# Kernel tuning notes

Measured on AMD Instinct MI355X. Metric: run time of the kernel, lower is better.

Reference implementation:

```python
import jax, jax.numpy as jnp
import numpy as np

B, C, N, K_NN = 16, 64, 2048, 3
OUT_C = 64


def setup_inputs() -> dict:
    key = jax.random.key(0)
    k1, k2, k3 = jax.random.split(key, 3)
    x = jax.random.normal(k1, (B, C, N), dtype=jnp.float32)
    fan_in = C * K_NN
    bound = 1.0 / np.sqrt(fan_in)
    W = jax.random.uniform(k2, (OUT_C, C, K_NN), minval=-bound, maxval=bound, dtype=jnp.float32)
    b = jax.random.uniform(k3, (OUT_C,), minval=-bound, maxval=bound, dtype=jnp.float32)
    return {"x": x, "W": W, "b": b}


def reference(x, W, b):
    # x: [B, C, N]; W: [O, C, K]; b: [O]
    K = W.shape[-1]
    # Pairwise squared distances: dist[b,i,j] = |x_i|^2 + |x_j|^2 - 2 x_i.x_j.
    # The original takes sqrt, but sqrt is monotone and the distances are only
    # used for top-k index selection, so we select on squared distances (same indices).
    norm_sq = jnp.sum(x * x, axis=1)                      # [B, N]
    dot = jnp.einsum('bcn,bcm->bnm', x, x)                # [B, N, N]
    dist_sq = norm_sq[:, :, None] + norm_sq[:, None, :] - 2.0 * dot  # [B, N, N]
    # K smallest distances per row -> neighbor indices [B, N, K]
    _, idx = jax.lax.top_k(-dist_sq, K)
    # Gather neighbors: neigh[b, c, n, k] = x[b, c, idx[b, n, k]]
    neigh = jax.vmap(lambda xb, ib: xb[:, ib])(x, idx)    # [B, C, N, K]
    # Conv1d with kernel_size == stride == K over the flattened [B, C, N*K]
    # tensor is exactly a per-window contraction over the K neighbors.
    out = jnp.einsum('bcnk,ock->bon', neigh, W) + b[None, :, None]  # [B, O, N]
    return out
```

## Files before the change

kernel.cpp:

```cpp
#include <hip/hip_runtime.h>
#include <cfloat>
#include <climits>

#define B_DIM 16
#define C_DIM 64
#define N_DIM 2048
#define O_DIM 64
#define K_NN  3

typedef __attribute__((ext_vector_type(8))) short bf16x8;
typedef __attribute__((ext_vector_type(4))) float floatx4;

#define GLDS16(gsrc, ldst)                                        \
  __builtin_amdgcn_global_load_lds(                               \
      (const __attribute__((address_space(1))) void*)(gsrc),      \
      (__attribute__((address_space(3))) void*)(ldst), 16, 0, 0)

__device__ __forceinline__ unsigned short f32_to_bf16_rne(float f) {
  unsigned int u = __float_as_uint(f);
  return (unsigned short)((u + 0x7fffu + ((u >> 16) & 1u)) >> 16);
}
__device__ __forceinline__ float bf16_to_f32(unsigned short h) {
  return __uint_as_float(((unsigned int)h) << 16);
}

__device__ __forceinline__ unsigned med3u(unsigned a, unsigned b, unsigned c) {
  unsigned mn = min(a, b), mx = max(a, b);
  return max(mn, min(mx, c));
}

__device__ __forceinline__ void ins4p(unsigned u, int jv, unsigned* k, int* j) {
  bool c3 = u < k[3], c2 = u < k[2], c1 = u < k[1], c0 = u < k[0];
  k[3] = c2 ? k[2] : (c3 ? u  : k[3]);
  j[3] = c2 ? j[2] : (c3 ? jv : j[3]);
  k[2] = c1 ? k[1] : (c2 ? u  : k[2]);
  j[2] = c1 ? j[1] : (c2 ? jv : j[2]);
  k[1] = c0 ? k[0] : (c1 ? u  : k[1]);
  j[1] = c0 ? j[0] : (c1 ? jv : j[1]);
  k[0] = c0 ? u  : k[0];
  j[0] = c0 ? jv : j[0];
}

__global__ __launch_bounds__(256) void prep_kernel(
    const float* __restrict__ x, float* __restrict__ xT,
    unsigned short* __restrict__ xTh, unsigned short* __restrict__ xTl,
    double* __restrict__ nd, float* __restrict__ nf,
    const float* __restrict__ W, float* __restrict__ Wt) {
  int bid = blockIdx.x;
  int t = threadIdx.x;
  if (bid >= 512) {
    int t2 = (bid - 512) * 256 + t;
    int o  = t2 / (C_DIM * K_NN);
    int ck = t2 - o * (C_DIM * K_NN);
    Wt[ck * O_DIM + o] = W[t2];
    return;
  }
  __shared__ __align__(16) float xs[C_DIM][68];
  int b  = bid >> 5;
  int n0 = (bid & 31) * 64;
  const float* xb = x + (size_t)b * C_DIM * N_DIM;
  #pragma unroll
  for (int r = 0; r < 4; ++r) {
    int idx = r * 256 + t;
    int c = idx >> 4;
    int qq = idx & 15;
    *(float4*)&xs[c][qq * 4] = *(const float4*)(xb + (size_t)c * N_DIM + n0 + qq * 4);
  }
  __syncthreads();
  int n = t >> 2, cg = t & 3;
  float v[16];
  #pragma unroll
  for (int cc = 0; cc < 16; ++cc) v[cc] = xs[cg * 16 + cc][n];
  double ps = 0.0;
  #pragma unroll
  for (int cc = 0; cc < 16; ++cc) ps = fma((double)v[cc], (double)v[cc], ps);
  ps += __shfl_xor(ps, 1, 64);
  ps += __shfl_xor(ps, 2, 64);
  size_t row = (size_t)b * N_DIM + n0 + n;
  #pragma unroll
  for (int qq = 0; qq < 4; ++qq) {
    float4 wv; wv.x = v[qq*4]; wv.y = v[qq*4+1]; wv.z = v[qq*4+2]; wv.w = v[qq*4+3];
    *(float4*)&xT[row * C_DIM + cg * 16 + qq * 4] = wv;
  }
  unsigned short hh[16], ll[16];
  #pragma unroll
  for (int cc = 0; cc < 16; ++cc) {
    hh[cc] = f32_to_bf16_rne(v[cc]);
    ll[cc] = f32_to_bf16_rne(v[cc] - bf16_to_f32(hh[cc]));
  }
  #pragma unroll
  for (int e = 0; e < 2; ++e) {
    int phys = (2 * cg + e) ^ (n & 7);
    unsigned int hp[4], lp[4];
    #pragma unroll
    for (int xk = 0; xk < 4; ++xk) {
      hp[xk] = (unsigned)hh[e*8 + 2*xk] | ((unsigned)hh[e*8 + 2*xk + 1] << 16);
      lp[xk] = (unsigned)ll[e*8 + 2*xk] | ((unsigned)ll[e*8 + 2*xk + 1] << 16);
    }
    ((uint4*)xTh)[row * 8 + phys] = *(uint4*)hp;
    ((uint4*)xTl)[row * 8 + phys] = *(uint4*)lp;
  }
  if (cg == 0) {
    nd[row] = ps;
    nf[row] = (float)ps + 512.0f;
  }
}

__global__ __launch_bounds__(256, 4) void topk_kernel(
    const unsigned short* __restrict__ xTh, const unsigned short* __restrict__ xTl,
    const float* __restrict__ nf, unsigned short* __restrict__ cand) {
  __shared__ __align__(16) unsigned short Jh[2][64 * 64];
  __shared__ __align__(16) unsigned short Jl[2][64 * 64];
  int bid   = blockIdx.x;
  bid = (bid & 7) * 128 + (bid >> 3);
  int q     = bid & 3;
  int itile = (bid >> 2) & 15;
  int b     = bid >> 6;
  int i0    = itile * 128;
  int jq0   = q * 512;
  int t = threadIdx.x;
  int w = t >> 6, lane = t & 63, quad = lane >> 4, col = lane & 15;
  int csw = col & 7;
  const unsigned short* xh = xTh + (size_t)b * N_DIM * 64;
  const unsigned short* xl = xTl + (size_t)b * N_DIM * 64;
  const float* nfb = nf + b * N_DIM;

  bf16x8 ih[2][2], il[2][2];
  #pragma unroll
  for (int s2 = 0; s2 < 2; ++s2) {
    #pragma unroll
    for (int ks = 0; ks < 2; ++ks) {
      size_t row = i0 + w * 32 + s2 * 16 + col;
      int phys = (ks * 4 + quad) ^ csw;
      ih[s2][ks] = *(const bf16x8*)(xh + row * 64 + phys * 8);
      il[s2][ks] = *(const bf16x8*)(xl + row * 64 + phys * 8);
    }
  }

  unsigned ck[2][4];
  #pragma unroll
  for (int s2 = 0; s2 < 2; ++s2)
    ck[s2][0] = ck[s2][1] = ck[s2][2] = ck[s2][3] = 0xFFFFFFFFu;

  int a0 = col * 64 + ((quad ^ csw) * 8);
  int a1 = col * 64 + (((4 + quad) ^ csw) * 8);

  const unsigned short* sbh = xh + (size_t)(jq0 + w * 16) * 64 + lane * 8;
  const unsigned short* sbl = xl + (size_t)(jq0 + w * 16) * 64 + lane * 8;
  int ldsb = w * 16 * 64;

  #pragma unroll
  for (int k2 = 0; k2 < 2; ++k2) {
    GLDS16(sbh + k2 * 512, &Jh[0][ldsb + k2 * 512]);
    GLDS16(sbl + k2 * 512, &Jl[0][ldsb + k2 * 512]);
  }
  __syncthreads();

  #pragma unroll
  for (int js = 0; js < 8; ++js) {
    int cur = js & 1, nxt = cur ^ 1;
    int j0 = jq0 + js * 64;

    if (js < 7) {
      #pragma unroll
      for (int k2 = 0; k2 < 2; ++k2) {
        GLDS16(sbh + (js + 1) * 4096 + k2 * 512, &Jh[nxt][ldsb + k2 * 512]);
        GLDS16(sbl + (js + 1) * 4096 + k2 * 512, &Jl[nxt][ldsb + k2 * 512]);
      }
    }

    floatx4 acc[2][4];
    #pragma unroll
    for (int s2 = 0; s2 < 2; ++s2)
      #pragma unroll
      for (int jt = 0; jt < 4; ++jt) acc[s2][jt] = (floatx4){0.f, 0.f, 0.f, 0.f};

    #pragma unroll
    for (int ks = 0; ks < 2; ++ks) {
      int ab = ks ? a1 : a0;
      #pragma unroll
      for (int jt = 0; jt < 4; ++jt) {
        bf16x8 jh = *(const bf16x8*)&Jh[cur][jt * 1024 + ab];
        bf16x8 jl = *(const bf16x8*)&Jl[cur][jt * 1024 + ab];
        #pragma unroll
        for (int s2 = 0; s2 < 2; ++s2) {
          acc[s2][jt] = __builtin_amdgcn_mfma_f32_16x16x32_bf16(jl, ih[s2][ks], acc[s2][jt], 0, 0, 0);
          acc[s2][jt] = __builtin_amdgcn_mfma_f32_16x16x32_bf16(jh, il[s2][ks], acc[s2][jt], 0, 0, 0);
          acc[s2][jt] = __builtin_amdgcn_mfma_f32_16x16x32_bf16(jh, ih[s2][ks], acc[s2][jt], 0, 0, 0);
        }
      }
    }

    unsigned locb = (unsigned)(js << 4);
    int jb = j0 + quad * 4;
    #pragma unroll
    for (int jt = 0; jt < 4; ++jt) {
      float4 nv = *(const float4*)(nfb + jb + jt * 16);
      float nfa[4] = {nv.x, nv.y, nv.z, nv.w};
      #pragma unroll
      for (int r = 0; r < 4; ++r) {
        unsigned idbits = locb | (unsigned)(jt * 4 + r);
        #pragma unroll
        for (int s2 = 0; s2 < 2; ++s2) {
          float key = fmaf(-2.0f, acc[s2][jt][r], nfa[r]);
          unsigned u = (__float_as_uint(key) & 0xFFFFFF80u) | idbits;
          unsigned m0 = min(ck[s2][0], u);
          unsigned m1 = med3u(ck[s2][0], u, ck[s2][1]);
          unsigned m2 = med3u(ck[s2][1], u, ck[s2][2]);
          unsigned m3 = med3u(ck[s2][2], u, ck[s2][3]);
          ck[s2][0] = m0; ck[s2][1] = m1; ck[s2][2] = m2; ck[s2][3] = m3;
        }
      }
    }

    __syncthreads();
  }

  #pragma unroll
  for (int s2 = 0; s2 < 2; ++s2) {
    int cj[4];
    unsigned cku[4];
    #pragma unroll
    for (int s = 0; s < 4; ++s) {
      unsigned loc = ck[s2][s] & 127u;
      cj[s] = jq0 + (int)((loc >> 4) << 6) + (int)(((loc >> 2) & 3u) << 4) +
              (quad << 2) + (int)(loc & 3u);
      cku[s] = ck[s2][s];
    }
    #pragma unroll
    for (int m = 16; m < 64; m <<= 1) {
      unsigned tu[4]; int tj[4];
      #pragma unroll
      for (int s = 0; s < 4; ++s) {
        tu[s] = __shfl_xor(cku[s], m, 64);
        tj[s] = __shfl_xor(cj[s], m, 64);
      }
      #pragma unroll
      for (int s = 0; s < 4; ++s) ins4p(tu[s], tj[s], cku, cj);
    }
    if (quad == 0) {
      int row = b * N_DIM + i0 + w * 32 + s2 * 16 + col;
      unsigned short* cp = cand + row * 16 + q * 4;
      cp[0] = (unsigned short)cj[0];
      cp[1] = (unsigned short)cj[1];
      cp[2] = (unsigned short)cj[2];
      cp[3] = (unsigned short)cj[3];
    }
  }
}

#define RNT 16
__global__ __launch_bounds__(256, 4) void refine_kernel(
    const float* __restrict__ xT, const double* __restrict__ nd,
    const unsigned short* __restrict__ cand,
    unsigned long long* __restrict__ tks_g) {
  __shared__ unsigned long long keys[RNT][17];
  int bid = blockIdx.x;
  bid = (bid & 7) * 256 + (bid >> 3);
  int b  = bid >> 7;
  int n0 = (bid & 127) * RNT;
  int t = threadIdx.x;
  int row = t >> 4, c = t & 15;
  int nn = n0 + row;
  int j = cand[(b * N_DIM + nn) * 16 + c];
  const float* xtb = xT + (size_t)b * N_DIM * C_DIM;
  const float* xn = xtb + (size_t)nn * C_DIM;
  const float* xj = xtb + (size_t)j * C_DIM;
  double nj = nd[b * N_DIM + j];

  double p[4];
  #pragma unroll
  for (int qq = 0; qq < 4; ++qq) {
    double s = 0.0;
    #pragma unroll
    for (int r = 0; r < 4; ++r) {
      float4 a  = *(const float4*)(xn + qq * 16 + r * 4);
      float4 bb = *(const float4*)(xj + qq * 16 + r * 4);
      s = fma((double)a.x, (double)bb.x, s);
      s = fma((double)a.y, (double)bb.y, s);
      s = fma((double)a.z, (double)bb.z, s);
      s = fma((double)a.w, (double)bb.w, s);
    }
    p[qq] = s;
  }
  double pd = (p[0] + p[1]) + (p[2] + p[3]);
  double key = fma(-2.0, pd, nj + 512.0);
  unsigned long long u =
      ((unsigned long long)__double_as_longlong(key) & ~2047ull) |
      (unsigned long long)(unsigned)j;
  keys[row][c] = u;
  __syncthreads();

  if (t < RNT) {
    unsigned long long k0 = ~0ull, k1 = ~0ull, k2 = ~0ull;
    #pragma unroll
    for (int s = 0; s < 16; ++s) {
      unsigned long long v = keys[t][s];
      bool c0 = v < k0, c1 = v < k1, c2 = v < k2;
      k2 = c1 ? k1 : (c2 ? v : k2);
      k1 = c0 ? k0 : (c1 ? v : k1);
      k0 = c0 ? v : k0;
    }
    tks_g[b * N_DIM + n0 + t] =
        (k0 & 2047ull) | ((k1 & 2047ull) << 16) | ((k2 & 2047ull) << 32);
  }
}

#define NT   64
#define NPAD 68
__global__ __launch_bounds__(256, 2) void conv_kernel(
    const float* __restrict__ xT, const unsigned long long* __restrict__ tks_g,
    const float* __restrict__ Wt, const float* __restrict__ bias,
    float* __restrict__ out) {
  __shared__ __align__(16) float nb[C_DIM * K_NN][NPAD];
  int bid = blockIdx.x;
  bid = (bid & 7) * 64 + (bid >> 3);
  int b  = bid >> 5;
  int n0 = (bid & 31) * NT;
  const float* xtb = xT + (size_t)b * N_DIM * C_DIM;
  int t = threadIdx.x;
  int w = t >> 6, lane = t & 63;

  unsigned long long t3 = tks_g[b * N_DIM + n0 + lane];

  #pragma unroll
  for (int p = 0; p < 12; ++p) {
    int h  = p * 4 + w;
    int k  = h >> 4;
    int sg = h & 15;
    int j = (int)((t3 >> (16 * k)) & 2047ull);
    float4 v = *(const float4*)(xtb + (size_t)j * C_DIM + sg * 4);
    nb[(sg * 4 + 0) * 3 + k][lane] = v.x;
    nb[(sg * 4 + 1) * 3 + k][lane] = v.y;
    nb[(sg * 4 + 2) * 3 + k][lane] = v.z;
    nb[(sg * 4 + 3) * 3 + k][lane] = v.w;
  }
  __syncthreads();

  int ng = t & 15, og = t >> 4;
  float acc[4][4];
  #pragma unroll
  for (int oo = 0; oo < 4; ++oo) {
    float bv = bias[(og << 2) + oo];
    #pragma unroll
    for (int nn2 = 0; nn2 < 4; ++nn2) acc[oo][nn2] = bv;
  }
  const float* nbp = &nb[0][0] + (ng << 2);
  const float* wtp = Wt + (og << 2);
  #pragma unroll 4
  for (int ckk = 0; ckk < C_DIM * K_NN; ++ckk) {
    float4 nv = *(const float4*)(nbp + ckk * NPAD);
    float4 wv = *(const float4*)(wtp + ckk * O_DIM);
    float na[4] = {nv.x, nv.y, nv.z, nv.w};
    float wa[4] = {wv.x, wv.y, wv.z, wv.w};
    #pragma unroll
    for (int oo = 0; oo < 4; ++oo)
      #pragma unroll
      for (int nn2 = 0; nn2 < 4; ++nn2)
        acc[oo][nn2] = fmaf(wa[oo], na[nn2], acc[oo][nn2]);
  }
  #pragma unroll
  for (int oo = 0; oo < 4; ++oo) {
    int o = (og << 2) + oo;
    float4 v; v.x = acc[oo][0]; v.y = acc[oo][1]; v.z = acc[oo][2]; v.w = acc[oo][3];
    *(float4*)&out[(size_t)(b * O_DIM + o) * N_DIM + n0 + (ng << 2)] = v;
  }
}

extern "C" void kernel_launch(void* const* d_in, const int* in_sizes, int n_in,
                              void* d_out, int out_size, void* d_ws, size_t ws_size,
                              hipStream_t stream) {
  const float* x    = (const float*)d_in[0];
  const float* W    = (const float*)d_in[1];
  const float* bias = (const float*)d_in[2];
  float* out = (float*)d_out;
  char* ws = (char*)d_ws;
  float*          xT  = (float*)ws;
  unsigned short* xTh = (unsigned short*)(ws + 8388608);
  unsigned short* xTl = (unsigned short*)(ws + 12582912);
  double*         nd  = (double*)(ws + 16777216);
  float*          nfp = (float*)(ws + 17039360);
  unsigned short* cd  = (unsigned short*)(ws + 17170432);
  float*          Wt  = (float*)(ws + 18219008);
  unsigned long long* tks = (unsigned long long*)(ws + 8388608);

  prep_kernel<<<512 + 48, 256, 0, stream>>>(x, xT, xTh, xTl, nd, nfp, W, Wt);
  topk_kernel<<<B_DIM * 16 * 4, 256, 0, stream>>>(xTh, xTl, nfp, cd);
  refine_kernel<<<B_DIM * (N_DIM / RNT), 256, 0, stream>>>(xT, nd, cd, tks);
  conv_kernel<<<B_DIM * (N_DIM / NT), 256, 0, stream>>>(xT, tks, Wt, bias, out);
}
```

Measured before the change: 149.6 us.

## Coalesce refine loads across lanes with shuffle reduction and drop XCD block swizzles

```diff
diff --git a/kernel.cpp b/kernel.cpp
--- a/kernel.cpp
+++ b/kernel.cpp
@@ -112,7 +112,6 @@
   __shared__ __align__(16) unsigned short Jh[2][64 * 64];
   __shared__ __align__(16) unsigned short Jl[2][64 * 64];
   int bid   = blockIdx.x;
-  bid = (bid & 7) * 128 + (bid >> 3);
   int q     = bid & 3;
   int itile = (bid >> 2) & 15;
   int b     = bid >> 6;
@@ -249,46 +248,44 @@
   }
 }
 
-#define RNT 16
+#define RNT 32
 __global__ __launch_bounds__(256, 4) void refine_kernel(
     const float* __restrict__ xT, const double* __restrict__ nd,
     const unsigned short* __restrict__ cand,
     unsigned long long* __restrict__ tks_g) {
   __shared__ unsigned long long keys[RNT][17];
   int bid = blockIdx.x;
-  bid = (bid & 7) * 256 + (bid >> 3);
-  int b  = bid >> 7;
-  int n0 = (bid & 127) * RNT;
+  int b  = bid >> 6;
+  int n0 = (bid & 63) * RNT;
   int t = threadIdx.x;
-  int row = t >> 4, c = t & 15;
-  int nn = n0 + row;
-  int j = cand[(b * N_DIM + nn) * 16 + c];
+  int w = t >> 6, lane = t & 63, quad = lane >> 4, ql = lane & 15;
   const float* xtb = xT + (size_t)b * N_DIM * C_DIM;
-  const float* xn = xtb + (size_t)nn * C_DIM;
-  const float* xj = xtb + (size_t)j * C_DIM;
-  double nj = nd[b * N_DIM + j];
-
-  double p[4];
-  #pragma unroll
-  for (int qq = 0; qq < 4; ++qq) {
-    double s = 0.0;
-    #pragma unroll
-    for (int r = 0; r < 4; ++r) {
-      float4 a  = *(const float4*)(xn + qq * 16 + r * 4);
-      float4 bb = *(const float4*)(xj + qq * 16 + r * 4);
-      s = fma((double)a.x, (double)bb.x, s);
-      s = fma((double)a.y, (double)bb.y, s);
-      s = fma((double)a.z, (double)bb.z, s);
-      s = fma((double)a.w, (double)bb.w, s);
-    }
-    p[qq] = s;
-  }
-  double pd = (p[0] + p[1]) + (p[2] + p[3]);
-  double key = fma(-2.0, pd, nj + 512.0);
-  unsigned long long u =
-      ((unsigned long long)__double_as_longlong(key) & ~2047ull) |
-      (unsigned long long)(unsigned)j;
-  keys[row][c] = u;
+  const double* ndb = nd + b * N_DIM;
+  const unsigned short* cb = cand + ((size_t)b * N_DIM + n0) * 16;
+  int c = w * 4 + quad;
+
+  #pragma unroll
+  for (int s = 0; s < RNT; ++s) {
+    int j = cb[s * 16 + c];
+    const float* xn = xtb + (size_t)(n0 + s) * C_DIM + ql * 4;
+    const float* xj = xtb + (size_t)j * C_DIM + ql * 4;
+    float4 a  = *(const float4*)xn;
+    float4 bb = *(const float4*)xj;
+    double pd = 0.0;
+    pd = fma((double)a.x, (double)bb.x, pd);
+    pd = fma((double)a.y, (double)bb.y, pd);
+    pd = fma((double)a.z, (double)bb.z, pd);
+    pd = fma((double)a.w, (double)bb.w, pd);
+    pd += __shfl_xor(pd, 1, 64);
+    pd += __shfl_xor(pd, 2, 64);
+    pd += __shfl_xor(pd, 4, 64);
+    pd += __shfl_xor(pd, 8, 64);
+    double key = fma(-2.0, pd, ndb[j] + 512.0);
+    unsigned long long u =
+        ((unsigned long long)__double_as_longlong(key) & ~2047ull) |
+        (unsigned long long)(unsigned)j;
+    if (ql == 0) keys[s][c] = u;
+  }
   __syncthreads();
 
   if (t < RNT) {
@@ -314,7 +311,6 @@
     float* __restrict__ out) {
   __shared__ __align__(16) float nb[C_DIM * K_NN][NPAD];
   int bid = blockIdx.x;
-  bid = (bid & 7) * 64 + (bid >> 3);
   int b  = bid >> 5;
   int n0 = (bid & 31) * NT;
   const float* xtb = xT + (size_t)b * N_DIM * C_DIM;
```

Result: slower. 159.0 us (+6.3%).
